# Optimization experiments

Hardware: AMD Instinct MI355X
Metric: run time of the kernel (lower is better)

Reference implementation:

```python
import jax, jax.numpy as jnp
import numpy as np

B, NPG, DEG = 512, 128, 16          # graphs, nodes/graph, out-degree
N = B * NPG                          # 65536 nodes
E = N * DEG                          # 1048576 edges
IN_DIM, HID, HEADS = 11, 32, 4
K1 = int(np.ceil(0.8 * NPG))         # 103 nodes/graph after pool1
K2 = int(np.ceil(0.8 * K1))          # 83 nodes/graph after pool2


def gat_conv(x, src, dst, mask, W, a_s, a_d, b, n_nodes):
    # PyG GATConv (concat=True, add_self_loops=True, eval mode -> no dropout)
    xp = (x @ W).reshape(n_nodes, HEADS, HID)            # [N,H,C]
    as_ = jnp.einsum('nhc,hc->nh', xp, a_s)
    ad_ = jnp.einsum('nhc,hc->nh', xp, a_d)
    loop = jnp.arange(n_nodes)
    s = jnp.concatenate([src, loop])
    d = jnp.concatenate([dst, loop])
    m = jnp.concatenate([mask, jnp.ones(n_nodes, bool)])
    logit = jax.nn.leaky_relu(as_[s] + ad_[d], 0.2)      # [E+N,H]
    logit = jnp.where(m[:, None], logit, -1e9)
    mx = jax.ops.segment_max(logit, d, num_segments=n_nodes)
    ex = jnp.exp(logit - mx[d]) * m[:, None]
    den = jax.ops.segment_sum(ex, d, num_segments=n_nodes)
    alpha = ex / (den[d] + 1e-16)                        # segment softmax over dst
    out = jax.ops.segment_sum(alpha[:, :, None] * xp[s], d, num_segments=n_nodes)
    return out.reshape(n_nodes, HEADS * HID) + b


def topk_pool(x, src, dst, mask, w, npg, k):
    # PyG TopKPooling: score = tanh((x*w).sum(-1)/||w||); keep top ceil(ratio*n) per graph
    nb = x.shape[0] // npg
    score = jnp.tanh((x @ w) / jnp.linalg.norm(w))
    vals, idx = jax.lax.top_k(score.reshape(nb, npg), k)  # [B,k]
    perm = (idx + (jnp.arange(nb) * npg)[:, None]).reshape(-1)
    x_new = x[perm] * vals.reshape(-1, 1)
    remap = jnp.full(nb * npg, -1).at[perm].set(jnp.arange(nb * k))
    ns, nd = remap[src], remap[dst]
    m = mask & (ns >= 0) & (nd >= 0)
    return x_new, jnp.where(m, ns, 0), jnp.where(m, nd, 0), m


def setup_inputs():
    key = jax.random.key(0)
    ks = jax.random.split(key, 24)
    s = 0.05
    x = jax.random.normal(ks[0], (N, IN_DIM), jnp.float32)
    src = jnp.repeat(jnp.arange(N), DEG)
    dst = (src // NPG) * NPG + jax.random.randint(ks[1], (E,), 0, NPG)
    edge_index = jnp.stack([src, dst])
    edge_attr = jax.random.normal(ks[2], (E, 4), jnp.float32)
    batch = jnp.repeat(jnp.arange(B), NPG)
    p = dict(
        W_g1=jax.random.normal(ks[3], (IN_DIM, HEADS * HID), jnp.float32) * s,
        att_src1=jax.random.normal(ks[4], (HEADS, HID), jnp.float32) * s,
        att_dst1=jax.random.normal(ks[5], (HEADS, HID), jnp.float32) * s,
        b_g1=jnp.zeros((HEADS * HID,), jnp.float32),
        W_t1=jax.random.normal(ks[6], (HEADS * HID, HID), jnp.float32) * s,
        b_t1=jnp.zeros((HID,), jnp.float32),
        pool_w1=jax.random.normal(ks[7], (HID,), jnp.float32) * s,
        W_g2=jax.random.normal(ks[8], (HID, HEADS * HID), jnp.float32) * s,
        att_src2=jax.random.normal(ks[9], (HEADS, HID), jnp.float32) * s,
        att_dst2=jax.random.normal(ks[10], (HEADS, HID), jnp.float32) * s,
        b_g2=jnp.zeros((HEADS * HID,), jnp.float32),
        W_t2=jax.random.normal(ks[11], (HEADS * HID, HID), jnp.float32) * s,
        b_t2=jnp.zeros((HID,), jnp.float32),
        pool_w2=jax.random.normal(ks[12], (HID,), jnp.float32) * s,
        W_l1=jax.random.normal(ks[13], (2 * HID, 256), jnp.float32) * s,
        b_l1=jnp.zeros((256,), jnp.float32),
        W_l2=jax.random.normal(ks[14], (256, 1024), jnp.float32) * s,
        b_l2=jnp.zeros((1024,), jnp.float32),
        W_l3=jax.random.normal(ks[15], (1024, 1), jnp.float32) * s,
        b_l3=jnp.zeros((1,), jnp.float32),
    )
    return dict(x=x, edge_index=edge_index, edge_attr=edge_attr, batch=batch, **p)


def reference(x, edge_index, edge_attr, batch,
              W_g1, att_src1, att_dst1, b_g1, W_t1, b_t1, pool_w1,
              W_g2, att_src2, att_dst2, b_g2, W_t2, b_t2, pool_w2,
              W_l1, b_l1, W_l2, b_l2, W_l3, b_l3):
    # edge_attr is ignored (GATConv built without edge_dim); batch is implicit
    # in the fixed equal-size graph layout.  Eval mode -> dropout disabled.
    src, dst = edge_index[0], edge_index[1]
    mask = jnp.ones(E, bool)
    h = jax.nn.relu(gat_conv(x, src, dst, mask, W_g1, att_src1, att_dst1, b_g1, N))
    h = h @ W_t1 + b_t1
    h, src, dst, mask = topk_pool(h, src, dst, mask, pool_w1, NPG, K1)
    h1 = h.reshape(B, K1, HID)
    g1 = jnp.concatenate([h1.max(1), h1.mean(1)], axis=1)   # [B, 2*HID]
    h = jax.nn.relu(gat_conv(h, src, dst, mask, W_g2, att_src2, att_dst2, b_g2, B * K1))
    h = h @ W_t2 + b_t2
    h, src, dst, mask = topk_pool(h, src, dst, mask, pool_w2, K1, K2)
    h2 = h.reshape(B, K2, HID)
    g2 = jnp.concatenate([h2.max(1), h2.mean(1)], axis=1)
    g = g1 + g2
    g = jax.nn.relu(g @ W_l1 + b_l1)
    g = jax.nn.relu(g @ W_l2 + b_l2)
    return g @ W_l3 + b_l3                                   # [B,1]
```

## Files before the change

kernel.cpp:

```cpp
#include <hip/hip_runtime.h>
#include <math.h>

constexpr int NPGc  = 128;
constexpr int NG    = 512;
constexpr int EPGc  = 2048;
constexpr int ETOT  = 1048576;
constexpr int IND   = 11;
constexpr int HIDc  = 32;
constexpr int FD    = 128;
constexpr int K1c   = 103;
constexpr int K2c   = 83;
constexpr int NN    = NG * NPGc;
constexpr int N2c   = NG * K1c;
constexpr int EPAD  = 2432;
constexpr int SBCAP = 2560;
constexpr int OFFSTR= 264;

__device__ __forceinline__ float lrelu(float x){ return fmaxf(x, 0.2f*x); }

__device__ __forceinline__ void agg4(const float4* __restrict__ X4, int r, int cbase, float e,
                                     float4& A0, float4& A1, float4& A2, float4& A3)
{
    int b = r * 8, s = r & 7;
    float4 u0 = X4[b + ((cbase+0) ^ s)];
    A0.x = fmaf(e, u0.x, A0.x); A0.y = fmaf(e, u0.y, A0.y); A0.z = fmaf(e, u0.z, A0.z); A0.w = fmaf(e, u0.w, A0.w);
    float4 u1 = X4[b + ((cbase+1) ^ s)];
    A1.x = fmaf(e, u1.x, A1.x); A1.y = fmaf(e, u1.y, A1.y); A1.z = fmaf(e, u1.z, A1.z); A1.w = fmaf(e, u1.w, A1.w);
    float4 u2 = X4[b + ((cbase+2) ^ s)];
    A2.x = fmaf(e, u2.x, A2.x); A2.y = fmaf(e, u2.y, A2.y); A2.z = fmaf(e, u2.z, A2.z); A2.w = fmaf(e, u2.w, A2.w);
    float4 u3 = X4[b + ((cbase+3) ^ s)];
    A3.x = fmaf(e, u3.x, A3.x); A3.y = fmaf(e, u3.y, A3.y); A3.z = fmaf(e, u3.z, A3.z); A3.w = fmaf(e, u3.w, A3.w);
}

template<int KIN>
__device__ void foldDev(const float* __restrict__ Wg, const float* __restrict__ avs,
                        const float* __restrict__ avd, float* __restrict__ S, float* __restrict__ D, int t)
{
    if (t < KIN * 4) {
        int k = t >> 2, h = t & 3;
        float s = 0.f, d = 0.f;
        for (int j = 0; j < HIDc; j++) {
            float w = Wg[k*FD + h*HIDc + j];
            s = fmaf(w, avs[h*HIDc + j], s);
            d = fmaf(w, avd[h*HIDc + j], d);
        }
        S[t] = s; D[t] = d;
    }
}

__global__ __launch_bounds__(256) void k_prep(const int* __restrict__ ei,
    const float* __restrict__ W1g, const float* __restrict__ s1, const float* __restrict__ d1,
    const float* __restrict__ W2g, const float* __restrict__ s2, const float* __restrict__ d2,
    int* __restrict__ csrOff, unsigned char* __restrict__ csrSB,
    float* __restrict__ S1, float* __restrict__ D1, float* __restrict__ S2, float* __restrict__ D2)
{
    int b = blockIdx.x, t = threadIdx.x;
    if (b >= NG) {
        if (b == NG)     foldDev<IND>(W1g, s1, d1, S1, D1, t);
        else             foldDev<HIDc>(W2g, s2, d2, S2, D2, t);
        return;
    }
    int g = b;
    __shared__ int cnt[128], cur[128], offL[129];
    __shared__ __align__(16) unsigned char sbL[SBCAP];
    const int FILL1 = (int)0x80808080u;
    if (t < 128) cnt[t] = 0;
    if (t < SBCAP/16) ((int4*)sbL)[t] = make_int4(FILL1, FILL1, FILL1, FILL1);
    __syncthreads();
    const int* dstG = ei + ETOT + g * EPGc;
    int dnv[8];
    #pragma unroll
    for (int q = 0; q < 8; q++) {
        int e = t + 256*q;
        dnv[q] = dstG[e] - g * NPGc;
        atomicAdd(&cnt[dnv[q]], 1);
    }
    __syncthreads();
    if (t < 64) {
        int c0 = cnt[2*t], c1 = cnt[2*t + 1];
        int p0 = (c0 + 3) & ~3, p1 = (c1 + 3) & ~3;
        int ps = p0 + p1, P = ps;
        #pragma unroll
        for (int dl = 1; dl < 64; dl <<= 1) { int v = __shfl_up(P, dl); if (t >= dl) P += v; }
        int E0 = P - ps;
        offL[2*t] = E0; offL[2*t + 1] = E0 + p0;
        cur[2*t]  = E0; cur[2*t + 1]  = E0 + p0;
        if (t == 63) offL[128] = P;
    }
    __syncthreads();
    #pragma unroll
    for (int q = 0; q < 8; q++) {
        int e = t + 256*q;
        int pos = atomicAdd(&cur[dnv[q]], 1);
        sbL[pos] = (unsigned char)(e >> 4);
    }
    __syncthreads();
    if (t < SBCAP/16) ((int4*)(csrSB + (size_t)g * SBCAP))[t] = ((const int4*)sbL)[t];
    if (t <= 128) csrOff[g*OFFSTR + t] = offL[t];
    if (t < 128)  csrOff[g*OFFSTR + 132 + t] = cur[t];
}

template<int NNODE, int KIN>
__global__ __launch_bounds__(256) void k_gat(
    const float* __restrict__ xin, const float* __restrict__ Wg,
    const float* __restrict__ WsS, const float* __restrict__ WsD,
    const int* __restrict__ csrOff, const unsigned char* __restrict__ csrSB,
    const float* __restrict__ bias, const float* __restrict__ Wt,
    float* __restrict__ htp)
{
    int g = blockIdx.x, h = blockIdx.y, t = threadIdx.x;
    __shared__ __align__(16) float xpL[NNODE * 32];
    __shared__ __align__(16) float WL[KIN * 32];
    __shared__ __align__(16) unsigned char sbL[SBCAP];
    __shared__ float asL[NNODE + 1], adL[NNODE], mL[NNODE], dIL[NNODE];
    __shared__ unsigned short offL[NNODE + 1];

    const float* xg = xin + (size_t)g * NNODE * KIN;

    for (int i = t; i < KIN * 32; i += 256) { int k = i >> 5, c = i & 31; WL[i] = Wg[k*FD + h*32 + c]; }
    if (t <= NNODE) offL[t] = (unsigned short)csrOff[g*OFFSTR + t];
    if (t < SBCAP/16) ((int4*)sbL)[t] = ((const int4*)(csrSB + (size_t)g * SBCAP))[t];
    if (t == 0) asL[NNODE] = -1e30f;
    __syncthreads();

    for (int p = t; p < NNODE * 8; p += 256) {
        int n = p >> 3, c4 = p & 7;
        float4 acc = make_float4(0.f, 0.f, 0.f, 0.f);
        if constexpr ((KIN & 3) == 0) {
            const float4* xr4 = (const float4*)(xg + (size_t)n * KIN);
            #pragma unroll
            for (int k4 = 0; k4 < KIN/4; k4++) {
                float4 xv = xr4[k4];
                float4 w;
                w = *(const float4*)&WL[(k4*4+0)*32 + c4*4];
                acc.x = fmaf(xv.x, w.x, acc.x); acc.y = fmaf(xv.x, w.y, acc.y); acc.z = fmaf(xv.x, w.z, acc.z); acc.w = fmaf(xv.x, w.w, acc.w);
                w = *(const float4*)&WL[(k4*4+1)*32 + c4*4];
                acc.x = fmaf(xv.y, w.x, acc.x); acc.y = fmaf(xv.y, w.y, acc.y); acc.z = fmaf(xv.y, w.z, acc.z); acc.w = fmaf(xv.y, w.w, acc.w);
                w = *(const float4*)&WL[(k4*4+2)*32 + c4*4];
                acc.x = fmaf(xv.z, w.x, acc.x); acc.y = fmaf(xv.z, w.y, acc.y); acc.z = fmaf(xv.z, w.z, acc.z); acc.w = fmaf(xv.z, w.w, acc.w);
                w = *(const float4*)&WL[(k4*4+3)*32 + c4*4];
                acc.x = fmaf(xv.w, w.x, acc.x); acc.y = fmaf(xv.w, w.y, acc.y); acc.z = fmaf(xv.w, w.z, acc.z); acc.w = fmaf(xv.w, w.w, acc.w);
            }
        } else {
            const float* xr = xg + (size_t)n * KIN;
            #pragma unroll
            for (int k = 0; k < KIN; k++) {
                float xv = xr[k];
                float4 w4 = *(const float4*)&WL[k*32 + c4*4];
                acc.x = fmaf(xv, w4.x, acc.x); acc.y = fmaf(xv, w4.y, acc.y);
                acc.z = fmaf(xv, w4.z, acc.z); acc.w = fmaf(xv, w4.w, acc.w);
            }
        }
        ((float4*)xpL)[n*8 + (c4 ^ (n & 7))] = acc;
    }
    if (t < NNODE) {
        const float* xr = xg + (size_t)t * KIN;
        float s = 0.f, d = 0.f;
        #pragma unroll
        for (int k = 0; k < KIN; k++) { float v = xr[k]; s = fmaf(v, WsS[k*4 + h], s); d = fmaf(v, WsD[k*4 + h], d); }
        asL[t] = s; adL[t] = d;
    }
    __syncthreads();

    if (t < NNODE) {
        float as_n = asL[t], adn = adL[t];
        int lo = offL[t], hi = offL[t + 1];
        float mx = as_n;
        for (int i = lo; i < hi; i += 4) {
            unsigned int q4 = *(const unsigned int*)(sbL + i);
            float a0 = asL[q4 & 255], a1 = asL[(q4 >> 8) & 255];
            float a2 = asL[(q4 >> 16) & 255], a3 = asL[q4 >> 24];
            mx = fmaxf(fmaxf(fmaxf(fmaxf(mx, a0), a1), a2), a3);
        }
        float m = lrelu(mx + adn);
        float den = expf(lrelu(as_n + adn) - m);
        for (int i = lo; i < hi; i += 4) {
            unsigned int q4 = *(const unsigned int*)(sbL + i);
            den += expf(lrelu(asL[q4 & 255] + adn) - m);
            den += expf(lrelu(asL[(q4 >> 8) & 255] + adn) - m);
            den += expf(lrelu(asL[(q4 >> 16) & 255] + adn) - m);
            den += expf(lrelu(asL[q4 >> 24] + adn) - m);
        }
        mL[t] = m; dIL[t] = 1.f / (den + 1e-16f);
    }
    __syncthreads();

    const float4* X4 = (const float4*)xpL;
    float4 A0, A1, A2, A3;
    int n = 0, cbase = 0;
    bool act = (t < NNODE * 2);
    if (act) {
        n = t >> 1; cbase = (t & 1) * 4;
        float adn = adL[n], mn = mL[n];
        float w0 = expf(lrelu(asL[n] + adn) - mn);
        int sw = n & 7, nb = n * 8;
        float4 v0 = X4[nb + ((cbase+0) ^ sw)];
        A0 = make_float4(w0*v0.x, w0*v0.y, w0*v0.z, w0*v0.w);
        float4 v1 = X4[nb + ((cbase+1) ^ sw)];
        A1 = make_float4(w0*v1.x, w0*v1.y, w0*v1.z, w0*v1.w);
        float4 v2 = X4[nb + ((cbase+2) ^ sw)];
        A2 = make_float4(w0*v2.x, w0*v2.y, w0*v2.z, w0*v2.w);
        float4 v3 = X4[nb + ((cbase+3) ^ sw)];
        A3 = make_float4(w0*v3.x, w0*v3.y, w0*v3.z, w0*v3.w);
        int lo = offL[n], hi = offL[n + 1];
        for (int s = lo; s < hi; s += 4) {
            unsigned int q4 = *(const unsigned int*)(sbL + s);
            int s0 = q4 & 255, s1 = (q4 >> 8) & 255, s2 = (q4 >> 16) & 255, s3 = q4 >> 24;
            float e0 = expf(lrelu(asL[s0] + adn) - mn);
            float e1 = expf(lrelu(asL[s1] + adn) - mn);
            float e2 = expf(lrelu(asL[s2] + adn) - mn);
            float e3 = expf(lrelu(asL[s3] + adn) - mn);
            agg4(X4, min(s0, NNODE-1), cbase, e0, A0, A1, A2, A3);
            agg4(X4, min(s1, NNODE-1), cbase, e1, A0, A1, A2, A3);
            agg4(X4, min(s2, NNODE-1), cbase, e2, A0, A1, A2, A3);
            agg4(X4, min(s3, NNODE-1), cbase, e3, A0, A1, A2, A3);
        }
        float inv = dIL[n];
        const float* bb = bias + h*32 + cbase*4;
        float4 b0 = *(const float4*)(bb);
        float4 b1 = *(const float4*)(bb + 4);
        float4 b2 = *(const float4*)(bb + 8);
        float4 b3 = *(const float4*)(bb + 12);
        A0.x = fmaxf(fmaf(A0.x, inv, b0.x), 0.f); A0.y = fmaxf(fmaf(A0.y, inv, b0.y), 0.f);
        A0.z = fmaxf(fmaf(A0.z, inv, b0.z), 0.f); A0.w = fmaxf(fmaf(A0.w, inv, b0.w), 0.f);
        A1.x = fmaxf(fmaf(A1.x, inv, b1.x), 0.f); A1.y = fmaxf(fmaf(A1.y, inv, b1.y), 0.f);
        A1.z = fmaxf(fmaf(A1.z, inv, b1.z), 0.f); A1.w = fmaxf(fmaf(A1.w, inv, b1.w), 0.f);
        A2.x = fmaxf(fmaf(A2.x, inv, b2.x), 0.f); A2.y = fmaxf(fmaf(A2.y, inv, b2.y), 0.f);
        A2.z = fmaxf(fmaf(A2.z, inv, b2.z), 0.f); A2.w = fmaxf(fmaf(A2.w, inv, b2.w), 0.f);
        A3.x = fmaxf(fmaf(A3.x, inv, b3.x), 0.f); A3.y = fmaxf(fmaf(A3.y, inv, b3.y), 0.f);
        A3.z = fmaxf(fmaf(A3.z, inv, b3.z), 0.f); A3.w = fmaxf(fmaf(A3.w, inv, b3.w), 0.f);
    }
    __syncthreads();
    if (act) {
        float4* X4w = (float4*)xpL;
        int sw = n & 7, nb = n * 8;
        X4w[nb + ((cbase+0) ^ sw)] = A0;
        X4w[nb + ((cbase+1) ^ sw)] = A1;
        X4w[nb + ((cbase+2) ^ sw)] = A2;
        X4w[nb + ((cbase+3) ^ sw)] = A3;
    }
    __syncthreads();

    {
        const int n0 = t >> 3, j4 = t & 7;
        const float* WtH = Wt + h*1024 + j4*4;
        #pragma unroll
        for (int rr = 0; rr < 4; rr++) {
            int nn = n0 + rr*32;
            if (nn < NNODE) {
                float4 acc = make_float4(0.f, 0.f, 0.f, 0.f);
                int sw = nn & 7, nb = nn * 8;
                #pragma unroll
                for (int c4 = 0; c4 < 8; c4++) {
                    float4 xv = X4[nb + (c4 ^ sw)];
                    float4 w;
                    w = *(const float4*)(WtH + (c4*4+0)*32);
                    acc.x = fmaf(xv.x, w.x, acc.x); acc.y = fmaf(xv.x, w.y, acc.y); acc.z = fmaf(xv.x, w.z, acc.z); acc.w = fmaf(xv.x, w.w, acc.w);
                    w = *(const float4*)(WtH + (c4*4+1)*32);
                    acc.x = fmaf(xv.y, w.x, acc.x); acc.y = fmaf(xv.y, w.y, acc.y); acc.z = fmaf(xv.y, w.z, acc.z); acc.w = fmaf(xv.y, w.w, acc.w);
                    w = *(const float4*)(WtH + (c4*4+2)*32);
                    acc.x = fmaf(xv.z, w.x, acc.x); acc.y = fmaf(xv.z, w.y, acc.y); acc.z = fmaf(xv.z, w.z, acc.z); acc.w = fmaf(xv.z, w.w, acc.w);
                    w = *(const float4*)(WtH + (c4*4+3)*32);
                    acc.x = fmaf(xv.w, w.x, acc.x); acc.y = fmaf(xv.w, w.y, acc.y); acc.z = fmaf(xv.w, w.z, acc.z); acc.w = fmaf(xv.w, w.w, acc.w);
                }
                *(float4*)(htp + ((size_t)(g * NNODE + nn) * 4 + h) * 32 + j4 * 4) = acc;
            }
        }
    }
}

template<int NIN, int KEEP, bool FIRST>
__global__ __launch_bounds__(512) void k_linpool(
    const float* __restrict__ htp, const float* __restrict__ bt, const float* __restrict__ pw,
    float* __restrict__ xnew, const int* __restrict__ ei,
    int* __restrict__ csrOffW, unsigned char* __restrict__ sbW,
    float* __restrict__ gfeat, const float* __restrict__ gprev,
    const float* __restrict__ W1, const float* __restrict__ b1,
    const float* __restrict__ W2, const float* __restrict__ b2,
    const float* __restrict__ W3, const float* __restrict__ b3,
    float* __restrict__ outp)
{
    int g = blockIdx.x, t = threadIdx.x;
    __shared__ float htL[NIN * 33];
    __shared__ float scoreL[NIN];
    __shared__ int rnkL[NIN];
    __shared__ int cnt[128], cur[128], offL[129];
    __shared__ __align__(16) unsigned char sbL[SBCAP];
    __shared__ float gvec[64];
    __shared__ float h1L[256], red[512];

    for (int p = t; p < NIN * 8; p += 512) {
        int n = p >> 3, q = p & 7;
        const float4* row = (const float4*)(htp + (size_t)(g * NIN + n) * 128);
        float4 s = ((const float4*)bt)[q];
        float4 p0 = row[q], p1 = row[8 + q], p2 = row[16 + q], p3 = row[24 + q];
        s.x += p0.x; s.y += p0.y; s.z += p0.z; s.w += p0.w;
        s.x += p1.x; s.y += p1.y; s.z += p1.z; s.w += p1.w;
        s.x += p2.x; s.y += p2.y; s.z += p2.z; s.w += p2.w;
        s.x += p3.x; s.y += p3.y; s.z += p3.z; s.w += p3.w;
        float* d = htL + n*33 + q*4;
        d[0] = s.x; d[1] = s.y; d[2] = s.z; d[3] = s.w;
    }
    __syncthreads();

    float nrm; { float ss = 0.f; for (int k = 0; k < HIDc; k++) { float w = pw[k]; ss = fmaf(w, w, ss); } nrm = sqrtf(ss); }
    if (t < NIN) {
        float dot = 0.f;
        for (int k = 0; k < HIDc; k++) dot = fmaf(htL[t*33 + k], pw[k], dot);
        scoreL[t] = tanhf(dot / nrm);
    }
    __syncthreads();
    if (t < NIN) {
        float si = scoreL[t]; int rank = 0;
        for (int q = 0; q < NIN; q++) {
            float sj = scoreL[q];
            rank += (sj > si || (sj == si && q < t)) ? 1 : 0;
        }
        rnkL[t] = (rank < KEEP) ? rank : -1;
    }
    __syncthreads();
    if constexpr (FIRST) {
        for (int p = t; p < NIN * 32; p += 512) {
            int n = p >> 5, jj = p & 31;
            int rk = rnkL[n];
            if (rk >= 0) xnew[((size_t)g*KEEP + rk)*HIDc + jj] = htL[n*33 + jj] * scoreL[n];
        }
    }
    if (t < HIDc) {
        float mx = -INFINITY, sm = 0.f;
        for (int n = 0; n < NIN; n++) {
            if (rnkL[n] >= 0) { float v = htL[n*33 + t] * scoreL[n]; mx = fmaxf(mx, v); sm += v; }
        }
        float mean = sm / (float)KEEP;
        if constexpr (FIRST) {
            gfeat[(size_t)g*64 + t]      = mx;
            gfeat[(size_t)g*64 + 32 + t] = mean;
        } else {
            gvec[t]      = gprev[(size_t)g*64 + t] + mx;
            gvec[32 + t] = gprev[(size_t)g*64 + 32 + t] + mean;
        }
    }

    if constexpr (FIRST) {
        __syncthreads();
        const int FILL2 = (int)0x67676767u;
        if (t < 128) cnt[t] = 0;
        if (t < SBCAP/16) ((int4*)sbL)[t] = make_int4(FILL2, FILL2, FILL2, FILL2);
        __syncthreads();
        const int* dstG = ei + ETOT + g * EPGc;
        int snv[4], dnv[4];
        #pragma unroll
        for (int q = 0; q < 4; q++) {
            int e = t + 512*q;
            int s = rnkL[e >> 4], d = rnkL[dstG[e] - g * NPGc];
            bool ok = (s >= 0 && d >= 0);
            snv[q] = s; dnv[q] = ok ? d : -1;
            if (ok) atomicAdd(&cnt[d], 1);
        }
        __syncthreads();
        if (t < 64) {
            int c0 = cnt[2*t], c1 = cnt[2*t + 1];
            int p0 = (c0 + 3) & ~3, p1 = (c1 + 3) & ~3;
            int ps = p0 + p1, P = ps;
            #pragma unroll
            for (int dl = 1; dl < 64; dl <<= 1) { int v = __shfl_up(P, dl); if (t >= dl) P += v; }
            int E0 = P - ps;
            offL[2*t] = E0; offL[2*t + 1] = E0 + p0;
            cur[2*t]  = E0; cur[2*t + 1]  = E0 + p0;
            if (t == 63) offL[128] = P;
        }
        __syncthreads();
        #pragma unroll
        for (int q = 0; q < 4; q++) {
            if (dnv[q] >= 0) {
                int pos = atomicAdd(&cur[dnv[q]], 1);
                sbL[pos] = (unsigned char)snv[q];
            }
        }
        __syncthreads();
        if (t < SBCAP/16) ((int4*)(sbW + (size_t)g * SBCAP))[t] = ((const int4*)sbL)[t];
        if (t <= K1c) csrOffW[g*OFFSTR + t] = offL[t];
        if (t < K1c)  csrOffW[g*OFFSTR + 132 + t] = cur[t];
    } else {
        __syncthreads();
        if (t < 256) {
            float a = b1[t];
            #pragma unroll 8
            for (int k = 0; k < 64; k++) a = fmaf(gvec[k], W1[k*256 + t], a);
            h1L[t] = fmaxf(a, 0.f);
        }
        __syncthreads();
        float2 bq = *(const float2*)(b2 + 2*t);
        float c0 = bq.x, c1 = bq.y;
        const float2* w2r = (const float2*)W2 + t;
        #pragma unroll 8
        for (int i = 0; i < 256; i++) {
            float hv = h1L[i];
            float2 w = w2r[(size_t)i * 512];
            c0 = fmaf(hv, w.x, c0);
            c1 = fmaf(hv, w.y, c1);
        }
        float2 w3q = *(const float2*)(W3 + 2*t);
        float p = fmaf(fmaxf(c0, 0.f), w3q.x, fmaxf(c1, 0.f) * w3q.y);
        red[t] = p;
        __syncthreads();
        for (int s = 256; s > 0; s >>= 1) { if (t < s) red[t] += red[t + s]; __syncthreads(); }
        if (t == 0) outp[g] = red[0] + b3[0];
    }
}

extern "C" void kernel_launch(void* const* d_in, const int* in_sizes, int n_in,
                              void* d_out, int out_size, void* d_ws, size_t ws_size,
                              hipStream_t stream)
{
    const float* x    = (const float*)d_in[0];
    const int*   ei   = (const int*)  d_in[1];
    const float* W_g1 = (const float*)d_in[4];
    const float* as1w = (const float*)d_in[5];
    const float* ad1w = (const float*)d_in[6];
    const float* b_g1 = (const float*)d_in[7];
    const float* W_t1 = (const float*)d_in[8];
    const float* b_t1 = (const float*)d_in[9];
    const float* pw1  = (const float*)d_in[10];
    const float* W_g2 = (const float*)d_in[11];
    const float* as2w = (const float*)d_in[12];
    const float* ad2w = (const float*)d_in[13];
    const float* b_g2 = (const float*)d_in[14];
    const float* W_t2 = (const float*)d_in[15];
    const float* b_t2 = (const float*)d_in[16];
    const float* pw2  = (const float*)d_in[17];
    const float* W_l1 = (const float*)d_in[18];
    const float* b_l1 = (const float*)d_in[19];
    const float* W_l2 = (const float*)d_in[20];
    const float* b_l2 = (const float*)d_in[21];
    const float* W_l3 = (const float*)d_in[22];
    const float* b_l3 = (const float*)d_in[23];
    float* out = (float*)d_out;

    char* ws = (char*)d_ws;
    size_t off = 0;
    auto alloc = [&](size_t bytes) -> void* {
        void* p = (void*)(ws + off);
        off += ((bytes + 255) / 256) * 256;
        return p;
    };
    float* htp1  = (float*)alloc((size_t)NN * 128 * 4);
    float* htp2  = (float*)alloc((size_t)N2c * 128 * 4);
    float* x2    = (float*)alloc((size_t)N2c * HIDc * 4);
    float* g1    = (float*)alloc((size_t)NG * 64 * 4);
    float* wsS1  = (float*)alloc(64 * 4);
    float* wsD1  = (float*)alloc(64 * 4);
    float* wsS2  = (float*)alloc(128 * 4);
    float* wsD2  = (float*)alloc(128 * 4);
    int*   off1  = (int*)  alloc((size_t)NG * OFFSTR * 4);
    unsigned char* sb1 = (unsigned char*)alloc((size_t)NG * SBCAP);
    int*   off2  = (int*)  alloc((size_t)NG * OFFSTR * 4);
    unsigned char* sb2 = (unsigned char*)alloc((size_t)NG * SBCAP);

    k_prep<<<NG + 2, 256, 0, stream>>>(ei, W_g1, as1w, ad1w, W_g2, as2w, ad2w,
                                       off1, sb1, wsS1, wsD1, wsS2, wsD2);

    k_gat<NPGc, IND><<<dim3(NG, 4), 256, 0, stream>>>(
        x, W_g1, wsS1, wsD1, off1, sb1, b_g1, W_t1, htp1);

    k_linpool<NPGc, K1c, true><<<NG, 512, 0, stream>>>(
        htp1, b_t1, pw1, x2, ei, off2, sb2, g1, nullptr,
        nullptr, nullptr, nullptr, nullptr, nullptr, nullptr, nullptr);

    k_gat<K1c, HIDc><<<dim3(NG, 4), 256, 0, stream>>>(
        x2, W_g2, wsS2, wsD2, off2, sb2, b_g2, W_t2, htp2);

    k_linpool<K1c, K2c, false><<<NG, 512, 0, stream>>>(
        htp2, b_t2, pw2, nullptr, nullptr, nullptr, nullptr, nullptr, g1,
        W_l1, b_l1, W_l2, b_l2, W_l3, b_l3, out);
}
```

Before: 291.2 us.

## Merge four per-head GAT blocks into one 1024-thread block per graph

The GAT kernel now launches one 1024-thread block per graph, with each 256-thread quarter handling one attention head, instead of a 2D grid of one block per (graph, head). The CSR offsets and source-byte lists are loaded into shared memory once per graph rather than four times. Shared memory grows roughly fourfold (per-head xp, attention and softmax arrays), which lowers the number of resident blocks per CU, and every barrier now spans 1024 threads. For the 11-wide input the weights are read straight from global memory instead of being staged in shared memory, and loop unrolling is reduced.

```diff
diff --git a/kernel.cpp b/kernel.cpp
--- a/kernel.cpp
+++ b/kernel.cpp
@@ -101,98 +101,113 @@
 }
 
 template<int NNODE, int KIN>
-__global__ __launch_bounds__(256) void k_gat(
+__global__ __launch_bounds__(1024) void k_gat(
     const float* __restrict__ xin, const float* __restrict__ Wg,
     const float* __restrict__ WsS, const float* __restrict__ WsD,
     const int* __restrict__ csrOff, const unsigned char* __restrict__ csrSB,
     const float* __restrict__ bias, const float* __restrict__ Wt,
     float* __restrict__ htp)
 {
-    int g = blockIdx.x, h = blockIdx.y, t = threadIdx.x;
-    __shared__ __align__(16) float xpL[NNODE * 32];
-    __shared__ __align__(16) float WL[KIN * 32];
+    const int g = blockIdx.x, t = threadIdx.x;
+    const int h = t >> 8, tt = t & 255;
+    constexpr bool STW = ((KIN & 3) == 0);
+    constexpr int WLSZ = STW ? 4 * KIN * 32 : 4;
+    __shared__ __align__(16) float xpL[4][NNODE * 32];
+    __shared__ __align__(16) float WL[WLSZ];
     __shared__ __align__(16) unsigned char sbL[SBCAP];
-    __shared__ float asL[NNODE + 1], adL[NNODE], mL[NNODE], dIL[NNODE];
+    __shared__ float asL[4][NNODE + 1], adL[4][NNODE], mL[4][NNODE], dIL[4][NNODE];
     __shared__ unsigned short offL[NNODE + 1];
 
-    const float* xg = xin + (size_t)g * NNODE * KIN;
-
-    for (int i = t; i < KIN * 32; i += 256) { int k = i >> 5, c = i & 31; WL[i] = Wg[k*FD + h*32 + c]; }
+    const float* xg  = xin + (size_t)g * NNODE * KIN;
+    const float* WgH = Wg + h*32;
+
     if (t <= NNODE) offL[t] = (unsigned short)csrOff[g*OFFSTR + t];
     if (t < SBCAP/16) ((int4*)sbL)[t] = ((const int4*)(csrSB + (size_t)g * SBCAP))[t];
-    if (t == 0) asL[NNODE] = -1e30f;
-    __syncthreads();
-
-    for (int p = t; p < NNODE * 8; p += 256) {
+    if (t < 4) asL[t][NNODE] = -1e30f;
+    if constexpr (STW) {
+        for (int i = t; i < 4*KIN*32; i += 1024) {
+            int hh = i >> 10;
+            int idx = i & 1023;
+            int k = idx >> 5, c = idx & 31;
+            WL[i] = Wg[k*FD + hh*32 + c];
+        }
+    }
+    __syncthreads();
+
+    float* xph = xpL[h];
+    for (int p = tt; p < NNODE * 8; p += 256) {
         int n = p >> 3, c4 = p & 7;
         float4 acc = make_float4(0.f, 0.f, 0.f, 0.f);
-        if constexpr ((KIN & 3) == 0) {
+        if constexpr (STW) {
             const float4* xr4 = (const float4*)(xg + (size_t)n * KIN);
-            #pragma unroll
+            const float* WH = WL + h*KIN*32;
+            #pragma unroll 2
             for (int k4 = 0; k4 < KIN/4; k4++) {
                 float4 xv = xr4[k4];
                 float4 w;
-                w = *(const float4*)&WL[(k4*4+0)*32 + c4*4];
+                w = *(const float4*)(WH + (k4*4+0)*32 + c4*4);
                 acc.x = fmaf(xv.x, w.x, acc.x); acc.y = fmaf(xv.x, w.y, acc.y); acc.z = fmaf(xv.x, w.z, acc.z); acc.w = fmaf(xv.x, w.w, acc.w);
-                w = *(const float4*)&WL[(k4*4+1)*32 + c4*4];
+                w = *(const float4*)(WH + (k4*4+1)*32 + c4*4);
                 acc.x = fmaf(xv.y, w.x, acc.x); acc.y = fmaf(xv.y, w.y, acc.y); acc.z = fmaf(xv.y, w.z, acc.z); acc.w = fmaf(xv.y, w.w, acc.w);
-                w = *(const float4*)&WL[(k4*4+2)*32 + c4*4];
+                w = *(const float4*)(WH + (k4*4+2)*32 + c4*4);
                 acc.x = fmaf(xv.z, w.x, acc.x); acc.y = fmaf(xv.z, w.y, acc.y); acc.z = fmaf(xv.z, w.z, acc.z); acc.w = fmaf(xv.z, w.w, acc.w);
-                w = *(const float4*)&WL[(k4*4+3)*32 + c4*4];
+                w = *(const float4*)(WH + (k4*4+3)*32 + c4*4);
                 acc.x = fmaf(xv.w, w.x, acc.x); acc.y = fmaf(xv.w, w.y, acc.y); acc.z = fmaf(xv.w, w.z, acc.z); acc.w = fmaf(xv.w, w.w, acc.w);
             }
         } else {
             const float* xr = xg + (size_t)n * KIN;
-            #pragma unroll
+            #pragma unroll 4
             for (int k = 0; k < KIN; k++) {
                 float xv = xr[k];
-                float4 w4 = *(const float4*)&WL[k*32 + c4*4];
+                float4 w4 = *(const float4*)(WgH + k*FD + c4*4);
                 acc.x = fmaf(xv, w4.x, acc.x); acc.y = fmaf(xv, w4.y, acc.y);
                 acc.z = fmaf(xv, w4.z, acc.z); acc.w = fmaf(xv, w4.w, acc.w);
             }
         }
-        ((float4*)xpL)[n*8 + (c4 ^ (n & 7))] = acc;
-    }
-    if (t < NNODE) {
-        const float* xr = xg + (size_t)t * KIN;
+        ((float4*)xph)[n*8 + (c4 ^ (n & 7))] = acc;
+    }
+    if (tt < NNODE) {
+        const float* xr = xg + (size_t)tt * KIN;
         float s = 0.f, d = 0.f;
         #pragma unroll
         for (int k = 0; k < KIN; k++) { float v = xr[k]; s = fmaf(v, WsS[k*4 + h], s); d = fmaf(v, WsD[k*4 + h], d); }
-        asL[t] = s; adL[t] = d;
-    }
-    __syncthreads();
-
-    if (t < NNODE) {
-        float as_n = asL[t], adn = adL[t];
-        int lo = offL[t], hi = offL[t + 1];
+        asL[h][tt] = s; adL[h][tt] = d;
+    }
+    __syncthreads();
+
+    if (tt < NNODE) {
+        const float* ash = asL[h];
+        float as_n = ash[tt], adn = adL[h][tt];
+        int lo = offL[tt], hi = offL[tt + 1];
         float mx = as_n;
         for (int i = lo; i < hi; i += 4) {
             unsigned int q4 = *(const unsigned int*)(sbL + i);
-            float a0 = asL[q4 & 255], a1 = asL[(q4 >> 8) & 255];
-            float a2 = asL[(q4 >> 16) & 255], a3 = asL[q4 >> 24];
+            float a0 = ash[q4 & 255], a1 = ash[(q4 >> 8) & 255];
+            float a2 = ash[(q4 >> 16) & 255], a3 = ash[q4 >> 24];
             mx = fmaxf(fmaxf(fmaxf(fmaxf(mx, a0), a1), a2), a3);
         }
         float m = lrelu(mx + adn);
         float den = expf(lrelu(as_n + adn) - m);
         for (int i = lo; i < hi; i += 4) {
             unsigned int q4 = *(const unsigned int*)(sbL + i);
-            den += expf(lrelu(asL[q4 & 255] + adn) - m);
-            den += expf(lrelu(asL[(q4 >> 8) & 255] + adn) - m);
-            den += expf(lrelu(asL[(q4 >> 16) & 255] + adn) - m);
-            den += expf(lrelu(asL[q4 >> 24] + adn) - m);
-        }
-        mL[t] = m; dIL[t] = 1.f / (den + 1e-16f);
-    }
-    __syncthreads();
-
-    const float4* X4 = (const float4*)xpL;
+            den += expf(lrelu(ash[q4 & 255] + adn) - m);
+            den += expf(lrelu(ash[(q4 >> 8) & 255] + adn) - m);
+            den += expf(lrelu(ash[(q4 >> 16) & 255] + adn) - m);
+            den += expf(lrelu(ash[q4 >> 24] + adn) - m);
+        }
+        mL[h][tt] = m; dIL[h][tt] = 1.f / (den + 1e-16f);
+    }
+    __syncthreads();
+
+    const float4* X4 = (const float4*)xpL[h];
     float4 A0, A1, A2, A3;
     int n = 0, cbase = 0;
-    bool act = (t < NNODE * 2);
+    bool act = (tt < NNODE * 2);
     if (act) {
-        n = t >> 1; cbase = (t & 1) * 4;
-        float adn = adL[n], mn = mL[n];
-        float w0 = expf(lrelu(asL[n] + adn) - mn);
+        const float* ash = asL[h];
+        n = tt >> 1; cbase = (tt & 1) * 4;
+        float adn = adL[h][n], mn = mL[h][n];
+        float w0 = expf(lrelu(ash[n] + adn) - mn);
         int sw = n & 7, nb = n * 8;
         float4 v0 = X4[nb + ((cbase+0) ^ sw)];
         A0 = make_float4(w0*v0.x, w0*v0.y, w0*v0.z, w0*v0.w);
@@ -206,16 +221,16 @@
         for (int s = lo; s < hi; s += 4) {
             unsigned int q4 = *(const unsigned int*)(sbL + s);
             int s0 = q4 & 255, s1 = (q4 >> 8) & 255, s2 = (q4 >> 16) & 255, s3 = q4 >> 24;
-            float e0 = expf(lrelu(asL[s0] + adn) - mn);
-            float e1 = expf(lrelu(asL[s1] + adn) - mn);
-            float e2 = expf(lrelu(asL[s2] + adn) - mn);
-            float e3 = expf(lrelu(asL[s3] + adn) - mn);
+            float e0 = expf(lrelu(ash[s0] + adn) - mn);
+            float e1 = expf(lrelu(ash[s1] + adn) - mn);
+            float e2 = expf(lrelu(ash[s2] + adn) - mn);
+            float e3 = expf(lrelu(ash[s3] + adn) - mn);
             agg4(X4, min(s0, NNODE-1), cbase, e0, A0, A1, A2, A3);
             agg4(X4, min(s1, NNODE-1), cbase, e1, A0, A1, A2, A3);
             agg4(X4, min(s2, NNODE-1), cbase, e2, A0, A1, A2, A3);
             agg4(X4, min(s3, NNODE-1), cbase, e3, A0, A1, A2, A3);
         }
-        float inv = dIL[n];
+        float inv = dIL[h][n];
         const float* bb = bias + h*32 + cbase*4;
         float4 b0 = *(const float4*)(bb);
         float4 b1 = *(const float4*)(bb + 4);
@@ -232,7 +247,7 @@
     }
     __syncthreads();
     if (act) {
-        float4* X4w = (float4*)xpL;
+        float4* X4w = (float4*)xpL[h];
         int sw = n & 7, nb = n * 8;
         X4w[nb + ((cbase+0) ^ sw)] = A0;
         X4w[nb + ((cbase+1) ^ sw)] = A1;
@@ -242,7 +257,7 @@
     __syncthreads();
 
     {
-        const int n0 = t >> 3, j4 = t & 7;
+        const int n0 = tt >> 3, j4 = tt & 7;
         const float* WtH = Wt + h*1024 + j4*4;
         #pragma unroll
         for (int rr = 0; rr < 4; rr++) {
@@ -460,14 +475,14 @@
     k_prep<<<NG + 2, 256, 0, stream>>>(ei, W_g1, as1w, ad1w, W_g2, as2w, ad2w,
                                        off1, sb1, wsS1, wsD1, wsS2, wsD2);
 
-    k_gat<NPGc, IND><<<dim3(NG, 4), 256, 0, stream>>>(
+    k_gat<NPGc, IND><<<NG, 1024, 0, stream>>>(
         x, W_g1, wsS1, wsD1, off1, sb1, b_g1, W_t1, htp1);
 
     k_linpool<NPGc, K1c, true><<<NG, 512, 0, stream>>>(
         htp1, b_t1, pw1, x2, ei, off2, sb2, g1, nullptr,
         nullptr, nullptr, nullptr, nullptr, nullptr, nullptr, nullptr);
 
-    k_gat<K1c, HIDc><<<dim3(NG, 4), 256, 0, stream>>>(
+    k_gat<K1c, HIDc><<<NG, 1024, 0, stream>>>(
         x2, W_g2, wsS2, wsD2, off2, sb2, b_g2, W_t2, htp2);
 
     k_linpool<K1c, K2c, false><<<NG, 512, 0, stream>>>(
```

Result: slower. 439.5 us (+50.9%).
